# Kernel optimization log

Hardware: AMD Instinct MI355X
Metric: run time of the kernel (lower is better)

The kernel has to match this reference:

```python
import jax, jax.numpy as jnp
import numpy as np

N = 100_000      # nodes
E = 3_200_000    # edges (before self-loops)
IN_DIM = 256
H1, H2 = 64, 32
OUT_DIM = 40
NEG_SLOPE = 0.2  # PyG GATConv default


def setup_inputs() -> dict:
    key = jax.random.key(0)
    ks = jax.random.split(key, 12)
    s = 0.05
    return {
        "x": jax.random.normal(ks[0], (N, IN_DIM), jnp.float32),
        "edge_index": jax.random.randint(ks[1], (2, E), 0, N, jnp.int32),
        "W1": jax.random.normal(ks[2], (IN_DIM, H1), jnp.float32) * s,
        "att_src1": jax.random.normal(ks[3], (H1,), jnp.float32) * s,
        "att_dst1": jax.random.normal(ks[4], (H1,), jnp.float32) * s,
        "b1": jnp.zeros((H1,), jnp.float32),
        "W2": jax.random.normal(ks[5], (H1, H2), jnp.float32) * s,
        "att_src2": jax.random.normal(ks[6], (H2,), jnp.float32) * s,
        "att_dst2": jax.random.normal(ks[7], (H2,), jnp.float32) * s,
        "b2": jnp.zeros((H2,), jnp.float32),
        "fcW": jax.random.normal(ks[8], (H2, OUT_DIM), jnp.float32) * s,
        "fcb": jnp.zeros((OUT_DIM,), jnp.float32),
    }


def gat_conv(x, src, dst, W, a_src, a_dst, b):
    """Single-head PyG GATConv (concat, heads=1). src/dst already include self-loops."""
    n = x.shape[0]
    h = x @ W                                   # [N, C] projected features (lin has no bias)
    alpha_s = (h * a_src).sum(-1)               # [N]
    alpha_d = (h * a_dst).sum(-1)               # [N]
    logit = jax.nn.leaky_relu(alpha_s[src] + alpha_d[dst], NEG_SLOPE)  # [E']
    # segment softmax over edges grouped by destination node
    m = jax.ops.segment_max(logit, dst, num_segments=n)               # [N]
    e = jnp.exp(logit - m[dst])                                        # [E']
    denom = jax.ops.segment_sum(e, dst, num_segments=n)               # [N]
    alpha = e / denom[dst]                                             # [E']
    out = jax.ops.segment_sum(h[src] * alpha[:, None], dst, num_segments=n)  # [N, C]
    return out + b


def reference(x, edge_index, W1, att_src1, att_dst1, b1, W2, att_src2, att_dst2, b2, fcW, fcb):
    n = x.shape[0]
    # add_self_loops=True (PyG GATConv default)
    loop = jnp.arange(n, dtype=edge_index.dtype)
    src = jnp.concatenate([edge_index[0], loop])
    dst = jnp.concatenate([edge_index[1], loop])
    h = jax.nn.relu(gat_conv(x, src, dst, W1, att_src1, att_dst1, b1))
    emb = jax.nn.relu(gat_conv(h, src, dst, W2, att_src2, att_dst2, b2))
    logits = emb @ fcW + fcb
    return emb, logits
```

## Files before the change

### kernel.cpp

```cpp
#include <hip/hip_runtime.h>
#include <hip/hip_bf16.h>

#define NEG_SLOPE 0.2f
#define IN_DIM 256
#define C1 64
#define C2 32
#define ODIM 40
#define SCAN_CHUNK 4096
#define BSHIFT 12
#define ECHUNK 8192
#define ECH2 16384
#define CH 10

typedef unsigned int uint32;
typedef unsigned short ushort16;

__device__ __forceinline__ unsigned bf16_rne(float f) {
    unsigned a = __float_as_uint(f);
    return (a + 0x7FFFu + ((a >> 16) & 1u)) >> 16;
}
__device__ __forceinline__ void bf16x2_unpack(unsigned u, float& f0, float& f1) {
    f0 = __uint_as_float(u << 16);
    f1 = __uint_as_float(u & 0xFFFF0000u);
}


__global__ void k_bhist(const int* __restrict__ dst, int E, int* __restrict__ gh,
                        int nblk, int nb) {
    __shared__ int h[32];
    int t = threadIdx.x;
    if (t < 32) h[t] = 0;
    __syncthreads();
    int base = blockIdx.x * ECHUNK;
    int end = min(base + ECHUNK, E);
    for (int i = base + t; i < end; i += 256) atomicAdd(&h[dst[i] >> BSHIFT], 1);
    __syncthreads();
    if (t < nb) gh[t * nblk + blockIdx.x] = h[t];
}

__global__ void k_bscan(int* __restrict__ gh, int L) {
    __shared__ int lds[256];
    __shared__ int carry;
    int t = threadIdx.x;
    if (t == 0) carry = 0;
    __syncthreads();
    for (int base = 0; base < L; base += 256) {
        int v = (base + t < L) ? gh[base + t] : 0;
        lds[t] = v; __syncthreads();
        for (int off = 1; off < 256; off <<= 1) {
            int u = (t >= off) ? lds[t - off] : 0;
            __syncthreads();
            lds[t] += u;
            __syncthreads();
        }
        if (base + t < L) gh[base + t] = lds[t] - v + carry;
        __syncthreads();
        if (t == 0) carry += lds[255];
        __syncthreads();
    }
}

__global__ void k_bplace(const int* __restrict__ src, const int* __restrict__ dst, int E,
                         const int* __restrict__ gh, int nblk, int nb,
                         int2* __restrict__ pairs) {
    __shared__ int cur[32];
    int t = threadIdx.x;
    if (t < nb) cur[t] = gh[t * nblk + blockIdx.x];
    __syncthreads();
    int base = blockIdx.x * ECHUNK;
    int end = min(base + ECHUNK, E);
    for (int i = base + t; i < end; i += 256) {
        int d = dst[i];
        int pos = atomicAdd(&cur[d >> BSHIFT], 1);
        pairs[pos] = make_int2(src[i], d);
    }
}

__device__ __forceinline__ void bc_map(int blk, int* b, int* c) {
    int xcd = blk & 7, k = blk >> 3;
    *b = (k & 3) * 8 + xcd;
    *c = k >> 2;
}

__global__ __launch_bounds__(512)
void k_nhist(const int2* __restrict__ pairs, const int* __restrict__ gh, int nblk,
             int nb, int E, int* __restrict__ chist) {
    __shared__ int h[4096];
    int b, c; bc_map(blockIdx.x, &b, &c);
    if (b >= nb) return;
    for (int i = threadIdx.x; i < 4096; i += 512) h[i] = 0;
    __syncthreads();
    int estart = gh[b * nblk];
    int eend = (b + 1 < nb) ? gh[(b + 1) * nblk] : E;
    int s0 = estart + c * ECH2;
    int s1 = min(s0 + ECH2, eend);
    for (int i = s0 + threadIdx.x; i < s1; i += 512)
        atomicAdd(&h[pairs[i].y & 4095], 1);
    __syncthreads();
    int* out = chist + ((size_t)b * CH + c) * 4096;
    for (int i = threadIdx.x; i < 4096; i += 512) out[i] = h[i];
}

__global__ void k_cnt(const int* __restrict__ chist, int* __restrict__ cnt, int n) {
    int i = blockIdx.x * 256 + threadIdx.x;
    if (i >= n) return;
    int b = i >> BSHIFT, j = i & 4095;
    const int* p = chist + ((size_t)b * CH) * 4096 + j;
    int s = 1;
#pragma unroll
    for (int c = 0; c < CH; c++) s += p[c * 4096];
    cnt[i] = s;
}

__global__ void k_scan1(const int* __restrict__ cnt, int n, int* __restrict__ bsums) {
    __shared__ int lds[256];
    int t = threadIdx.x;
    int base = blockIdx.x * SCAN_CHUNK + t * 16;
    int s = 0;
#pragma unroll
    for (int i = 0; i < 16; i++) { int idx = base + i; s += (idx < n) ? cnt[idx] : 0; }
    lds[t] = s; __syncthreads();
    for (int off = 128; off > 0; off >>= 1) {
        if (t < off) lds[t] += lds[t + off];
        __syncthreads();
    }
    if (t == 0) bsums[blockIdx.x] = lds[0];
}

__global__ void k_scan2(int* bsums, int nb, int* row_ptr, int n, int total) {
    __shared__ int lds[256];
    int t = threadIdx.x;
    int v = (t < nb) ? bsums[t] : 0;
    lds[t] = v; __syncthreads();
    for (int off = 1; off < 256; off <<= 1) {
        int u = (t >= off) ? lds[t - off] : 0;
        __syncthreads();
        lds[t] += u;
        __syncthreads();
    }
    if (t < nb) bsums[t] = lds[t] - v;
    if (t == 0) row_ptr[n] = total;
}

__global__ void k_scan3(const int* __restrict__ cnt, int n, const int* __restrict__ bsums,
                        int* __restrict__ row_ptr) {
    __shared__ int lds[256];
    int t = threadIdx.x;
    int base = blockIdx.x * SCAN_CHUNK + t * 16;
    int loc[16];
    int s = 0;
#pragma unroll
    for (int i = 0; i < 16; i++) {
        int idx = base + i;
        int c = (idx < n) ? cnt[idx] : 0;
        loc[i] = s; s += c;
    }
    lds[t] = s; __syncthreads();
    for (int off = 1; off < 256; off <<= 1) {
        int u = (t >= off) ? lds[t - off] : 0;
        __syncthreads();
        lds[t] += u;
        __syncthreads();
    }
    int texcl = lds[t] - s + bsums[blockIdx.x];
#pragma unroll
    for (int i = 0; i < 16; i++) {
        int idx = base + i;
        if (idx < n) row_ptr[idx] = texcl + loc[i];
    }
}

__global__ void k_selfloop(const int* __restrict__ row_ptr, int n, int* __restrict__ adj) {
    int i = blockIdx.x * 256 + threadIdx.x;
    if (i < n) adj[row_ptr[i]] = i;
}

__global__ void k_nscan(int* __restrict__ chist, const int* __restrict__ row_ptr, int n) {
    int i = blockIdx.x * 256 + threadIdx.x;
    if (i >= n) return;
    int b = i >> BSHIFT, j = i & 4095;
    int* p = chist + ((size_t)b * CH) * 4096 + j;
    int s = row_ptr[i] + 1;
#pragma unroll
    for (int c = 0; c < CH; c++) { int t = p[c * 4096]; p[c * 4096] = s; s += t; }
}

__global__ __launch_bounds__(512)
void k_place2(const int2* __restrict__ pairs, const int* __restrict__ gh, int nblk,
              int nb, int E, const int* __restrict__ chist, int* __restrict__ adj) {
    __shared__ int cur[4096];
    int b, c; bc_map(blockIdx.x, &b, &c);
    if (b >= nb) return;
    const int* cs = chist + ((size_t)b * CH + c) * 4096;
    for (int i = threadIdx.x; i < 4096; i += 512) cur[i] = cs[i];
    __syncthreads();
    int estart = gh[b * nblk];
    int eend = (b + 1 < nb) ? gh[(b + 1) * nblk] : E;
    int s0 = estart + c * ECH2;
    int s1 = min(s0 + ECH2, eend);
    for (int i = s0 + threadIdx.x; i < s1; i += 512) {
        int2 p = pairs[i];
        int pos = atomicAdd(&cur[p.y & 4095], 1);
        adj[pos] = p.x;
    }
}


__global__ __launch_bounds__(256, 4)
void k_gemm1(const float* __restrict__ x, const float* __restrict__ W1,
             const float* __restrict__ attS, const float* __restrict__ attD,
             ushort16* __restrict__ h1b, float* __restrict__ as1,
             float* __restrict__ ad1, int n) {
    int row = blockIdx.x * 256 + threadIdx.x;
    bool active = row < n;
    int rowc = active ? row : n - 1;
    const float4* xr = (const float4*)(x + (size_t)rowc * IN_DIM);

    float acc[64];
#pragma unroll
    for (int c = 0; c < 64; c++) acc[c] = 0.f;

#define FMA_K(XC, KK) { \
        const float* wk = wb + (KK) * C1; \
        _Pragma("unroll") \
        for (int c = 0; c < 64; c++) acc[c] = fmaf((XC), wk[c], acc[c]); }

    for (int k0 = 0; k0 < 16; k0++) {
        float4 xv0 = xr[k0 * 4 + 0];
        float4 xv1 = xr[k0 * 4 + 1];
        float4 xv2 = xr[k0 * 4 + 2];
        float4 xv3 = xr[k0 * 4 + 3];
        const float* wb = W1 + (size_t)(k0 * 16) * C1;
        FMA_K(xv0.x, 0)  FMA_K(xv0.y, 1)  FMA_K(xv0.z, 2)  FMA_K(xv0.w, 3)
        FMA_K(xv1.x, 4)  FMA_K(xv1.y, 5)  FMA_K(xv1.z, 6)  FMA_K(xv1.w, 7)
        FMA_K(xv2.x, 8)  FMA_K(xv2.y, 9)  FMA_K(xv2.z, 10) FMA_K(xv2.w, 11)
        FMA_K(xv3.x, 12) FMA_K(xv3.y, 13) FMA_K(xv3.z, 14) FMA_K(xv3.w, 15)
    }
#undef FMA_K

    if (!active) return;
    float vs = 0.f, vd = 0.f;
#pragma unroll
    for (int c = 0; c < 64; c++) {
        vs = fmaf(acc[c], attS[c], vs);
        vd = fmaf(acc[c], attD[c], vd);
    }
    as1[row] = vs; ad1[row] = vd;

    uint4* hp = (uint4*)(h1b + (size_t)row * C1);
#pragma unroll
    for (int j = 0; j < 8; j++) {
        unsigned p0 = bf16_rne(acc[j*8+0]) | (bf16_rne(acc[j*8+1]) << 16);
        unsigned p1 = bf16_rne(acc[j*8+2]) | (bf16_rne(acc[j*8+3]) << 16);
        unsigned p2 = bf16_rne(acc[j*8+4]) | (bf16_rne(acc[j*8+5]) << 16);
        unsigned p3 = bf16_rne(acc[j*8+6]) | (bf16_rne(acc[j*8+7]) << 16);
        hp[j] = make_uint4(p0, p1, p2, p3);
    }
}


__global__ __launch_bounds__(256)
void k_agg1(const ushort16* __restrict__ h1b, const float* __restrict__ as1,
            const float* __restrict__ ad1, const int* __restrict__ row_ptr,
            const int* __restrict__ adj, const float* __restrict__ b1,
            float* __restrict__ h1out, int n) {
    int wave = (blockIdx.x * 256 + threadIdx.x) >> 6;
    int lane = threadIdx.x & 63;
    if (wave >= n) return;
    int d = wave;
    int beg = row_ptr[d], end = row_ptr[d + 1];
    float adv = ad1[d];
    int g = lane >> 3, cq = lane & 7;
    float acc[8];
#pragma unroll
    for (int k = 0; k < 8; k++) acc[k] = 0.f;
    float dsum = 0.f;

#define AGG1_ROUND(E_) { \
        int se = __shfl(s, (E_)); \
        float we = __shfl(w, (E_)); \
        uint4 u = ((const uint4*)(h1b + (size_t)se * C1))[cq]; \
        float f0, f1; \
        bf16x2_unpack(u.x, f0, f1); acc[0]=fmaf(we,f0,acc[0]); acc[1]=fmaf(we,f1,acc[1]); \
        bf16x2_unpack(u.y, f0, f1); acc[2]=fmaf(we,f0,acc[2]); acc[3]=fmaf(we,f1,acc[3]); \
        bf16x2_unpack(u.z, f0, f1); acc[4]=fmaf(we,f0,acc[4]); acc[5]=fmaf(we,f1,acc[5]); \
        bf16x2_unpack(u.w, f0, f1); acc[6]=fmaf(we,f0,acc[6]); acc[7]=fmaf(we,f1,acc[7]); }

    for (int base = beg; base < end; base += 64) {
        int cnt = min(64, end - base);
        int s = d; float w = 0.f;
        if (lane < cnt) {
            s = adj[base + lane];
            float lg = as1[s] + adv;
            lg = lg > 0.f ? lg : NEG_SLOPE * lg;
            w = expf(lg);
            dsum += w;
        }
        int j = 0;
        for (; j + 32 <= cnt; j += 32) {
            AGG1_ROUND(j + g)
            AGG1_ROUND(j + 8 + g)
            AGG1_ROUND(j + 16 + g)
            AGG1_ROUND(j + 24 + g)
        }
        for (; j < cnt; j += 8) AGG1_ROUND(j + g)
    }
#undef AGG1_ROUND

#pragma unroll
    for (int off = 32; off > 0; off >>= 1) dsum += __shfl_xor(dsum, off);
#pragma unroll
    for (int off = 8; off <= 32; off <<= 1) {
#pragma unroll
        for (int k = 0; k < 8; k++) acc[k] += __shfl_xor(acc[k], off);
    }
    if (g == 0) {
        float inv = 1.f / dsum;
        float4 bv0 = ((const float4*)b1)[cq * 2];
        float4 bv1 = ((const float4*)b1)[cq * 2 + 1];
        float4 o0, o1;
        o0.x = acc[0] * inv + bv0.x; o0.x = o0.x > 0.f ? o0.x : 0.f;
        o0.y = acc[1] * inv + bv0.y; o0.y = o0.y > 0.f ? o0.y : 0.f;
        o0.z = acc[2] * inv + bv0.z; o0.z = o0.z > 0.f ? o0.z : 0.f;
        o0.w = acc[3] * inv + bv0.w; o0.w = o0.w > 0.f ? o0.w : 0.f;
        o1.x = acc[4] * inv + bv1.x; o1.x = o1.x > 0.f ? o1.x : 0.f;
        o1.y = acc[5] * inv + bv1.y; o1.y = o1.y > 0.f ? o1.y : 0.f;
        o1.z = acc[6] * inv + bv1.z; o1.z = o1.z > 0.f ? o1.z : 0.f;
        o1.w = acc[7] * inv + bv1.w; o1.w = o1.w > 0.f ? o1.w : 0.f;
        float4* op = (float4*)(h1out + (size_t)d * C1 + cq * 8);
        op[0] = o0; op[1] = o1;
    }
}


__global__ __launch_bounds__(256)
void k_gemm2(const float* __restrict__ h1out, const float* __restrict__ W2,
             const float* __restrict__ attS, const float* __restrict__ attD,
             ushort16* __restrict__ h2b, float* __restrict__ as2,
             float* __restrict__ ad2, int n) {
    __shared__ float w2t[C2 * 68];
    __shared__ float sAttS[C2], sAttD[C2];
    int t = threadIdx.x;
    for (int i = t; i < C1 * C2; i += 256) {
        int k = i >> 5, c = i & 31;
        w2t[c * 68 + k] = W2[i];
    }
    if (t < C2) { sAttS[t] = attS[t]; sAttD[t] = attD[t]; }
    __syncthreads();
    int wave = t >> 6, lane = t & 63;
    int col = lane & 31, half = lane >> 5;
    int rowbase = blockIdx.x * 32 + wave * 8;
    const float* wrow = &w2t[col * 68];
    for (int rr = 0; rr < 8; rr += 2) {
        int row = rowbase + rr + half;
        if (row >= n) return;
        float acc = 0.f;
#pragma unroll
        for (int k = 0; k < C1; k += 4) {
            float4 wv = *(const float4*)&wrow[k];
            float4 xv = *(const float4*)&h1out[(size_t)row * C1 + k];
            acc = fmaf(xv.x, wv.x, acc);
            acc = fmaf(xv.y, wv.y, acc);
            acc = fmaf(xv.z, wv.z, acc);
            acc = fmaf(xv.w, wv.w, acc);
        }
        h2b[(size_t)row * C2 + col] = (ushort16)bf16_rne(acc);
        float vs = acc * sAttS[col], vd = acc * sAttD[col];
#pragma unroll
        for (int off = 16; off > 0; off >>= 1) {
            vs += __shfl_xor(vs, off);
            vd += __shfl_xor(vd, off);
        }
        if (col == 0) { as2[row] = vs; ad2[row] = vd; }
    }
}


__global__ __launch_bounds__(256)
void k_agg2(const ushort16* __restrict__ h2b, const float* __restrict__ as2,
            const float* __restrict__ ad2, const int* __restrict__ row_ptr,
            const int* __restrict__ adj, const float* __restrict__ b2,
            float* __restrict__ emb, int n) {
    int wave = (blockIdx.x * 256 + threadIdx.x) >> 6;
    int lane = threadIdx.x & 63;
    if (wave >= n) return;
    int d = wave;
    int beg = row_ptr[d], end = row_ptr[d + 1];
    float adv = ad2[d];
    int g = lane >> 2, cq = lane & 3;
    float acc[8];
#pragma unroll
    for (int k = 0; k < 8; k++) acc[k] = 0.f;
    float dsum = 0.f;

#define AGG2_ROUND(E_) { \
        int se = __shfl(s, (E_)); \
        float we = __shfl(w, (E_)); \
        uint4 u = ((const uint4*)(h2b + (size_t)se * C2))[cq]; \
        float f0, f1; \
        bf16x2_unpack(u.x, f0, f1); acc[0]=fmaf(we,f0,acc[0]); acc[1]=fmaf(we,f1,acc[1]); \
        bf16x2_unpack(u.y, f0, f1); acc[2]=fmaf(we,f0,acc[2]); acc[3]=fmaf(we,f1,acc[3]); \
        bf16x2_unpack(u.z, f0, f1); acc[4]=fmaf(we,f0,acc[4]); acc[5]=fmaf(we,f1,acc[5]); \
        bf16x2_unpack(u.w, f0, f1); acc[6]=fmaf(we,f0,acc[6]); acc[7]=fmaf(we,f1,acc[7]); }

    for (int base = beg; base < end; base += 64) {
        int cnt = min(64, end - base);
        int s = d; float w = 0.f;
        if (lane < cnt) {
            s = adj[base + lane];
            float lg = as2[s] + adv;
            lg = lg > 0.f ? lg : NEG_SLOPE * lg;
            w = expf(lg);
            dsum += w;
        }
        int j = 0;
        for (; j + 64 <= cnt; j += 64) {
            AGG2_ROUND(j + g)
            AGG2_ROUND(j + 16 + g)
            AGG2_ROUND(j + 32 + g)
            AGG2_ROUND(j + 48 + g)
        }
        for (; j < cnt; j += 16) AGG2_ROUND(j + g)
    }
#undef AGG2_ROUND

#pragma unroll
    for (int off = 32; off > 0; off >>= 1) dsum += __shfl_xor(dsum, off);
#pragma unroll
    for (int off = 4; off <= 32; off <<= 1) {
#pragma unroll
        for (int k = 0; k < 8; k++) acc[k] += __shfl_xor(acc[k], off);
    }
    if (g == 0) {
        float inv = 1.f / dsum;
        float4 bv0 = ((const float4*)b2)[cq * 2];
        float4 bv1 = ((const float4*)b2)[cq * 2 + 1];
        float4 o0, o1;
        o0.x = acc[0] * inv + bv0.x; o0.x = o0.x > 0.f ? o0.x : 0.f;
        o0.y = acc[1] * inv + bv0.y; o0.y = o0.y > 0.f ? o0.y : 0.f;
        o0.z = acc[2] * inv + bv0.z; o0.z = o0.z > 0.f ? o0.z : 0.f;
        o0.w = acc[3] * inv + bv0.w; o0.w = o0.w > 0.f ? o0.w : 0.f;
        o1.x = acc[4] * inv + bv1.x; o1.x = o1.x > 0.f ? o1.x : 0.f;
        o1.y = acc[5] * inv + bv1.y; o1.y = o1.y > 0.f ? o1.y : 0.f;
        o1.z = acc[6] * inv + bv1.z; o1.z = o1.z > 0.f ? o1.z : 0.f;
        o1.w = acc[7] * inv + bv1.w; o1.w = o1.w > 0.f ? o1.w : 0.f;
        float4* op = (float4*)(emb + (size_t)d * C2 + cq * 8);
        op[0] = o0; op[1] = o1;
    }
}


__global__ __launch_bounds__(256)
void k_logits(const float* __restrict__ emb, const float* __restrict__ fcW,
              const float* __restrict__ fcb, float* __restrict__ out, int n) {
    __shared__ float w[C2 * ODIM];
    __shared__ float b[ODIM];
    int t = threadIdx.x;
    for (int i = t; i < C2 * ODIM; i += 256) w[i] = fcW[i];
    if (t < ODIM) b[t] = fcb[t];
    __syncthreads();
    int lane = t & 63;
    int row = blockIdx.x * 4 + (t >> 6);
    if (row >= n) return;
    float acc = (lane < ODIM) ? b[lane] : 0.f;
    const float4* er = (const float4*)&emb[(size_t)row * C2];
#pragma unroll
    for (int c4 = 0; c4 < 8; c4++) {
        float4 e = er[c4];
        int c = c4 * 4;
        if (lane < ODIM) {
            acc = fmaf(e.x, w[(c + 0) * ODIM + lane], acc);
            acc = fmaf(e.y, w[(c + 1) * ODIM + lane], acc);
            acc = fmaf(e.z, w[(c + 2) * ODIM + lane], acc);
            acc = fmaf(e.w, w[(c + 3) * ODIM + lane], acc);
        }
    }
    if (lane < ODIM) out[(size_t)row * ODIM + lane] = acc;
}


extern "C" void kernel_launch(void* const* d_in, const int* in_sizes, int n_in,
                              void* d_out, int out_size, void* d_ws, size_t ws_size,
                              hipStream_t stream) {
    const float* x    = (const float*)d_in[0];
    const int*   ei   = (const int*)d_in[1];
    const float* W1   = (const float*)d_in[2];
    const float* aS1  = (const float*)d_in[3];
    const float* aD1  = (const float*)d_in[4];
    const float* b1   = (const float*)d_in[5];
    const float* W2   = (const float*)d_in[6];
    const float* aS2  = (const float*)d_in[7];
    const float* aD2  = (const float*)d_in[8];
    const float* b2   = (const float*)d_in[9];
    const float* fcW  = (const float*)d_in[10];
    const float* fcb  = (const float*)d_in[11];

    const int N = in_sizes[0] / IN_DIM;
    const int E = in_sizes[1] / 2;
    const int* src = ei;
    const int* dst = ei + E;

    ushort16* h1b = (ushort16*)d_ws;
    float* h1out  = (float*)((char*)d_ws + (size_t)N * C1 * 2);
    float* as1    = h1out + (size_t)N * C1;
    float* ad1    = as1 + N;
    float* as2    = ad1 + N;
    float* ad2    = as2 + N;
    int*   cnt    = (int*)(ad2 + N);
    int*   row_ptr = cnt + N;
    int*   bsums   = row_ptr + (N + 1);
    int*   adj     = bsums + 256;
    int*   gh      = adj + (E + N);

    int2* pairs = (int2*)h1out;
    int*  chist = (int*)h1b;
    ushort16* h2b = (ushort16*)h1b;

    float* emb    = (float*)d_out;
    float* logits = emb + (size_t)N * C2;

    int nbN   = (N + 255) / 256;
    int nbS   = (N + SCAN_CHUNK - 1) / SCAN_CHUNK;
    int nblkE = (E + ECHUNK - 1) / ECHUNK;
    int nb    = (N + (1 << BSHIFT) - 1) >> BSHIFT;
    int nBC   = 8 * 4 * CH;

    k_bhist<<<nblkE, 256, 0, stream>>>(dst, E, gh, nblkE, nb);
    k_bscan<<<1, 256, 0, stream>>>(gh, nb * nblkE);
    k_bplace<<<nblkE, 256, 0, stream>>>(src, dst, E, gh, nblkE, nb, pairs);
    k_nhist<<<nBC, 512, 0, stream>>>(pairs, gh, nblkE, nb, E, chist);
    k_cnt<<<nbN, 256, 0, stream>>>(chist, cnt, N);
    k_scan1<<<nbS, 256, 0, stream>>>(cnt, N, bsums);
    k_scan2<<<1, 256, 0, stream>>>(bsums, nbS, row_ptr, N, E + N);
    k_scan3<<<nbS, 256, 0, stream>>>(cnt, N, bsums, row_ptr);
    k_selfloop<<<nbN, 256, 0, stream>>>(row_ptr, N, adj);
    k_nscan<<<nbN, 256, 0, stream>>>(chist, row_ptr, N);
    k_place2<<<nBC, 512, 0, stream>>>(pairs, gh, nblkE, nb, E, chist, adj);

    k_gemm1<<<nbN, 256, 0, stream>>>(x, W1, aS1, aD1, h1b, as1, ad1, N);
    int nbA = (N + 3) / 4;
    k_agg1<<<nbA, 256, 0, stream>>>(h1b, as1, ad1, row_ptr, adj, b1, h1out, N);
    int nbG2 = (N + 31) / 32;
    k_gemm2<<<nbG2, 256, 0, stream>>>(h1out, W2, aS2, aD2, h2b, as2, ad2, N);
    k_agg2<<<nbA, 256, 0, stream>>>(h2b, as2, ad2, row_ptr, adj, b2, emb, N);
    k_logits<<<nbA, 256, 0, stream>>>(emb, fcW, fcb, logits, N);
}
```

Measured before the change: 457.1 us.

## Restructure first GEMM as lane-per-column with W1 tiles staged in LDS

The first projection kernel no longer has each thread own a whole row with 64 accumulators reading W1 from global memory. Each wave now handles 8 rows with one output column per lane, and W1 is staged in 64-row tiles in shared memory. Attention dot products become wave shuffle reductions, and bf16 outputs are written one element per lane. The goal is lower register pressure and better reuse of W1, at the cost of broadcast x loads repeated across all lanes, block barriers, and narrower stores.

```diff
diff --git a/kernel.cpp b/kernel.cpp
--- a/kernel.cpp
+++ b/kernel.cpp
@@ -12,7 +12,6 @@
 #define ECH2 16384
 #define CH 10
 
-typedef unsigned int uint32;
 typedef unsigned short ushort16;
 
 __device__ __forceinline__ unsigned bf16_rne(float f) {
@@ -211,50 +210,59 @@
              const float* __restrict__ attS, const float* __restrict__ attD,
              ushort16* __restrict__ h1b, float* __restrict__ as1,
              float* __restrict__ ad1, int n) {
-    int row = blockIdx.x * 256 + threadIdx.x;
-    bool active = row < n;
-    int rowc = active ? row : n - 1;
-    const float4* xr = (const float4*)(x + (size_t)rowc * IN_DIM);
-
-    float acc[64];
-#pragma unroll
-    for (int c = 0; c < 64; c++) acc[c] = 0.f;
-
-#define FMA_K(XC, KK) { \
-        const float* wk = wb + (KK) * C1; \
-        _Pragma("unroll") \
-        for (int c = 0; c < 64; c++) acc[c] = fmaf((XC), wk[c], acc[c]); }
-
-    for (int k0 = 0; k0 < 16; k0++) {
-        float4 xv0 = xr[k0 * 4 + 0];
-        float4 xv1 = xr[k0 * 4 + 1];
-        float4 xv2 = xr[k0 * 4 + 2];
-        float4 xv3 = xr[k0 * 4 + 3];
-        const float* wb = W1 + (size_t)(k0 * 16) * C1;
-        FMA_K(xv0.x, 0)  FMA_K(xv0.y, 1)  FMA_K(xv0.z, 2)  FMA_K(xv0.w, 3)
-        FMA_K(xv1.x, 4)  FMA_K(xv1.y, 5)  FMA_K(xv1.z, 6)  FMA_K(xv1.w, 7)
-        FMA_K(xv2.x, 8)  FMA_K(xv2.y, 9)  FMA_K(xv2.z, 10) FMA_K(xv2.w, 11)
-        FMA_K(xv3.x, 12) FMA_K(xv3.y, 13) FMA_K(xv3.z, 14) FMA_K(xv3.w, 15)
-    }
-#undef FMA_K
-
-    if (!active) return;
-    float vs = 0.f, vd = 0.f;
-#pragma unroll
-    for (int c = 0; c < 64; c++) {
-        vs = fmaf(acc[c], attS[c], vs);
-        vd = fmaf(acc[c], attD[c], vd);
-    }
-    as1[row] = vs; ad1[row] = vd;
-
-    uint4* hp = (uint4*)(h1b + (size_t)row * C1);
-#pragma unroll
-    for (int j = 0; j < 8; j++) {
-        unsigned p0 = bf16_rne(acc[j*8+0]) | (bf16_rne(acc[j*8+1]) << 16);
-        unsigned p1 = bf16_rne(acc[j*8+2]) | (bf16_rne(acc[j*8+3]) << 16);
-        unsigned p2 = bf16_rne(acc[j*8+4]) | (bf16_rne(acc[j*8+5]) << 16);
-        unsigned p3 = bf16_rne(acc[j*8+6]) | (bf16_rne(acc[j*8+7]) << 16);
-        hp[j] = make_uint4(p0, p1, p2, p3);
+    __shared__ float wt[64 * C1];
+    int t = threadIdx.x;
+    int wave = t >> 6, lane = t & 63;
+    int row0 = blockIdx.x * 32 + wave * 8;
+
+    const float* xr[8];
+#pragma unroll
+    for (int r = 0; r < 8; r++) {
+        int row = row0 + r; if (row >= n) row = n - 1;
+        xr[r] = x + (size_t)row * IN_DIM;
+    }
+    float acc[8];
+#pragma unroll
+    for (int r = 0; r < 8; r++) acc[r] = 0.f;
+    float aS = attS[lane], aD = attD[lane];
+
+    for (int k0 = 0; k0 < IN_DIM; k0 += 64) {
+        if (k0) __syncthreads();
+#pragma unroll
+        for (int i = 0; i < 16; i++) {
+            int flat = i * 256 + t;
+            wt[flat] = W1[k0 * C1 + flat];
+        }
+        __syncthreads();
+        for (int kq = 0; kq < 16; kq++) {
+            float w0 = wt[(kq * 4 + 0) * C1 + lane];
+            float w1 = wt[(kq * 4 + 1) * C1 + lane];
+            float w2 = wt[(kq * 4 + 2) * C1 + lane];
+            float w3 = wt[(kq * 4 + 3) * C1 + lane];
+#pragma unroll
+            for (int r = 0; r < 8; r++) {
+                float4 xv = *(const float4*)&xr[r][k0 + kq * 4];
+                acc[r] = fmaf(xv.x, w0, acc[r]);
+                acc[r] = fmaf(xv.y, w1, acc[r]);
+                acc[r] = fmaf(xv.z, w2, acc[r]);
+                acc[r] = fmaf(xv.w, w3, acc[r]);
+            }
+        }
+    }
+
+#pragma unroll
+    for (int r = 0; r < 8; r++) {
+        int row = row0 + r;
+        if (row >= n) break;
+        float h = acc[r];
+        h1b[(size_t)row * C1 + lane] = (ushort16)bf16_rne(h);
+        float vs = h * aS, vd = h * aD;
+#pragma unroll
+        for (int off = 32; off > 0; off >>= 1) {
+            vs += __shfl_xor(vs, off);
+            vd += __shfl_xor(vd, off);
+        }
+        if (lane == 0) { as1[row] = vs; ad1[row] = vd; }
     }
 }
 
@@ -537,7 +545,8 @@
     k_nscan<<<nbN, 256, 0, stream>>>(chist, row_ptr, N);
     k_place2<<<nBC, 512, 0, stream>>>(pairs, gh, nblkE, nb, E, chist, adj);
 
-    k_gemm1<<<nbN, 256, 0, stream>>>(x, W1, aS1, aD1, h1b, as1, ad1, N);
+    int nbG1 = (N + 31) / 32;
+    k_gemm1<<<nbG1, 256, 0, stream>>>(x, W1, aS1, aD1, h1b, as1, ad1, N);
     int nbA = (N + 3) / 4;
     k_agg1<<<nbA, 256, 0, stream>>>(h1b, as1, ad1, row_ptr, adj, b1, h1out, N);
     int nbG2 = (N + 31) / 32;
```

Measured after the change: 545.9 us. 1.19x slower.
